# Performance work log

Measured on AMD Instinct MI355X. Metric: run time of the kernel, lower is better.

## Reference

```python
import jax, jax.numpy as jnp
import numpy as np

EMBED_DIM = 1024
NUM_HEADS = 16
HEAD_DIM = EMBED_DIM // NUM_HEADS  # 64
KERNEL_SIZE = 64


def apply_rotary_emb(x, freqs_cos, freqs_sin):
    # x: [B, L, H, D]; freqs: [L, D//2]
    x_r = x[..., 0::2]
    x_i = x[..., 1::2]
    cos = freqs_cos[None, :, None, :]
    sin = freqs_sin[None, :, None, :]
    out_r = x_r * cos - x_i * sin
    out_i = x_r * sin + x_i * cos
    return jnp.stack([out_r, out_i], axis=-1).reshape(x.shape)


def setup_inputs() -> dict:
    key = jax.random.key(0)
    ks = jax.random.split(key, 8)
    B, L = 4, 4096
    x = jax.random.normal(ks[0], (B, L, EMBED_DIM), dtype=jnp.float32)
    freqs_cos = jax.random.normal(ks[1], (L, HEAD_DIM // 2), dtype=jnp.float32)
    freqs_sin = jax.random.normal(ks[2], (L, HEAD_DIM // 2), dtype=jnp.float32)
    attention_mask = jnp.ones((B, L), dtype=jnp.float32)
    scale = 1.0 / np.sqrt(EMBED_DIM)
    Wqkv = jax.random.normal(ks[3], (EMBED_DIM, 3 * EMBED_DIM), dtype=jnp.float32) * scale
    bqkv = jnp.zeros((3 * EMBED_DIM,), dtype=jnp.float32)
    proj = jax.random.normal(ks[4], (NUM_HEADS, HEAD_DIM, KERNEL_SIZE), dtype=jnp.float32) / np.sqrt(HEAD_DIM)
    Wout = jax.random.normal(ks[5], (EMBED_DIM, EMBED_DIM), dtype=jnp.float32) * scale
    bout = jnp.zeros((EMBED_DIM,), dtype=jnp.float32)
    return {"x": x, "freqs_cos": freqs_cos, "freqs_sin": freqs_sin,
            "attention_mask": attention_mask, "Wqkv": Wqkv, "bqkv": bqkv,
            "proj": proj, "Wout": Wout, "bout": bout}


def reference(x, freqs_cos, freqs_sin, attention_mask, Wqkv, bqkv, proj, Wout, bout):
    B, L, E = x.shape
    H, D = NUM_HEADS, HEAD_DIM
    qkv = x @ Wqkv + bqkv  # [B, L, 3E]
    q, k, v = jnp.split(qkv, 3, axis=-1)
    q = q.reshape(B, L, H, D)
    k = k.reshape(B, L, H, D)
    v = v.reshape(B, L, H, D)
    q = apply_rotary_emb(q, freqs_cos, freqs_sin)
    k = apply_rotary_emb(k, freqs_cos, freqs_sin)
    q = q.transpose(0, 2, 1, 3)  # [B, H, L, D]
    k = k.transpose(0, 2, 1, 3)
    v = v.transpose(0, 2, 1, 3)
    q_prime = jax.nn.relu(jnp.einsum('bhld,hdm->bhlm', q, proj))
    k_prime = jax.nn.relu(jnp.einsum('bhld,hdm->bhlm', k, proj))
    mask = attention_mask[:, None, :, None]  # [B, 1, L, 1]
    k_prime = k_prime * mask
    v = v * mask
    kv = jnp.einsum('bhlm,bhld->bhmd', k_prime, v)      # [B, H, M, D]
    context = jnp.einsum('bhlm,bhmd->bhld', q_prime, kv)  # [B, H, L, D]
    k_sum = k_prime.sum(axis=2)  # [B, H, M]
    norm = jnp.einsum('bhlm,bhm->bhl', q_prime, k_sum)
    output = context / (norm[..., None] + 0.0001)
    output = output.transpose(0, 2, 1, 3).reshape(B, L, E)
    return output @ Wout + bout
```

## Files before the change

### kernel.cpp

```cpp
#include <hip/hip_runtime.h>

#define LSEQ   4096
#define ROWS   16384
#define EMBED  1024
#define NHEADS 16
#define HDIM   64
#define QKV_N  3072

typedef __attribute__((ext_vector_type(8))) short bf16x8;
typedef __attribute__((ext_vector_type(8))) unsigned short u16x8;
typedef __attribute__((ext_vector_type(4))) float f32x4;

__device__ inline unsigned short bf16_rne(float x) {
    unsigned int u = __float_as_uint(x);
    unsigned int r = (u + 0x7fffu + ((u >> 16) & 1u)) >> 16;
    return (unsigned short)r;
}
__device__ inline float bf16_to_f32(unsigned short h) {
    return __uint_as_float(((unsigned int)h) << 16);
}

__device__ __forceinline__ int swz64(int row, int s) {
    return row * 64 + ((((s >> 3) ^ (row & 7))) << 3) + (s & 7);
}

__global__ __launch_bounds__(256)
void convert_hilo(const float* __restrict__ in, unsigned short* __restrict__ hi,
                  unsigned short* __restrict__ lo, int n)
{
    int i = (blockIdx.x * 256 + threadIdx.x) << 2;
    if (i >= n) return;
    float4 v = *reinterpret_cast<const float4*>(&in[i]);
    float a[4] = {v.x, v.y, v.z, v.w};
    unsigned short hh[4], ll[4];
    #pragma unroll
    for (int j = 0; j < 4; ++j) {
        hh[j] = bf16_rne(a[j]);
        ll[j] = bf16_rne(a[j] - bf16_to_f32(hh[j]));
    }
    *reinterpret_cast<ushort4*>(&hi[i]) = make_ushort4(hh[0], hh[1], hh[2], hh[3]);
    *reinterpret_cast<ushort4*>(&lo[i]) = make_ushort4(ll[0], ll[1], ll[2], ll[3]);
}

__global__ __launch_bounds__(256)
void convert_T_hilo(const float* __restrict__ in, unsigned short* __restrict__ hi,
                    unsigned short* __restrict__ lo, int K, int N)
{
    __shared__ float tile[64][65];
    const int n0 = blockIdx.x * 64, k0 = blockIdx.y * 64;
    const int t = threadIdx.x;
    #pragma unroll
    for (int i = 0; i < 16; ++i) {
        int idx = t + i * 256;
        int r = idx >> 6, c = idx & 63;
        tile[r][c] = in[(size_t)(k0 + r) * N + n0 + c];
    }
    __syncthreads();
    #pragma unroll
    for (int i = 0; i < 16; ++i) {
        int idx = t + i * 256;
        int r = idx >> 6, c = idx & 63;
        float v = tile[c][r];
        unsigned short h = bf16_rne(v);
        unsigned short l = bf16_rne(v - bf16_to_f32(h));
        size_t o = (size_t)(n0 + r) * K + k0 + c;
        hi[o] = h;
        lo[o] = l;
    }
}

__global__ __launch_bounds__(512)
void gemm3_kernel(const unsigned short* __restrict__ Ah, const unsigned short* __restrict__ Al,
                  const unsigned short* __restrict__ Bh, const unsigned short* __restrict__ Bl,
                  const float* __restrict__ bias, float* __restrict__ C,
                  int K, int ldc)
{
    __shared__ __align__(16) unsigned short lds[2][32768];

    const int t = threadIdx.x;
    const int wave = t >> 6, lane = t & 63;
    const int wr = wave >> 2, wc = wave & 3;
    const int fr = lane & 15, fq = lane >> 4;

    const int nwg = gridDim.x * gridDim.y;
    const int wg  = blockIdx.y * gridDim.x + blockIdx.x;
    const int swz = (wg & 7) * (nwg >> 3) + (wg >> 3);
    const int bx = swz % gridDim.x, by = swz / gridDim.x;
    const int rowBase = by * 256;
    const int colBase = bx * 256;

    const int op = wave >> 1;
    const unsigned short* src = (op == 0) ? Ah : (op == 1) ? Al : (op == 2) ? Bh : Bl;
    const int tileRow0 = ((wave < 4) ? rowBase : colBase) + (wave & 1) * 128;
    const int subOff = op * 8192 + (wave & 1) * 4096;
    const int sRow = lane >> 2;
    const int sChunk = (((lane & 3) ^ ((lane >> 3) & 3)) << 3);

    f32x4 acc[8][4] = {};
    const int NT = K >> 5;

    #pragma unroll
    for (int i = 0; i < 8; ++i) {
        const unsigned short* g = src + (size_t)(tileRow0 + i * 16 + sRow) * K + sChunk;
        __builtin_amdgcn_global_load_lds(
            (const __attribute__((address_space(1))) void*)g,
            (__attribute__((address_space(3))) void*)&lds[0][subOff + i * 512], 16, 0, 0);
    }
    __syncthreads();

    for (int tI = 0; tI < NT; ++tI) {
        const int cur = tI & 1;
        const unsigned short* ldsC = lds[cur];
        const int k0 = (tI + 1) << 5;
        const bool pref = (tI + 1 < NT);

        bf16x8 bhf[4], blf[4];

        #pragma unroll
        for (int p = 0; p < 4; ++p) {
            if (pref && p < 2) {
                const int i0 = p * 4;
                #pragma unroll
                for (int i = 0; i < 4; ++i) {
                    const unsigned short* g =
                        src + (size_t)(tileRow0 + (i0 + i) * 16 + sRow) * K + k0 + sChunk;
                    __builtin_amdgcn_global_load_lds(
                        (const __attribute__((address_space(1))) void*)g,
                        (__attribute__((address_space(3))) void*)&lds[cur ^ 1][subOff + (i0 + i) * 512], 16, 0, 0);
                }
            }

            bf16x8 ahf[2], alf[2];
            #pragma unroll
            for (int mm = 0; mm < 2; ++mm) {
                int m = p * 2 + mm;
                int r = wr * 128 + m * 16 + fr;
                int off = r * 32 + ((fq ^ ((r >> 1) & 3)) << 3);
                ahf[mm] = *reinterpret_cast<const bf16x8*>(&ldsC[off]);
                alf[mm] = *reinterpret_cast<const bf16x8*>(&ldsC[8192 + off]);
            }
            if (p == 0) {
                #pragma unroll
                for (int n = 0; n < 4; ++n) {
                    int rb = wc * 64 + n * 16 + fr;
                    int off = rb * 32 + ((fq ^ ((rb >> 1) & 3)) << 3);
                    bhf[n] = *reinterpret_cast<const bf16x8*>(&ldsC[16384 + off]);
                    blf[n] = *reinterpret_cast<const bf16x8*>(&ldsC[24576 + off]);
                }
            }

            __builtin_amdgcn_s_barrier();
            asm volatile("s_waitcnt lgkmcnt(0)" ::: "memory");
            __builtin_amdgcn_sched_barrier(0);
            __builtin_amdgcn_s_setprio(1);
            #pragma unroll
            for (int mm = 0; mm < 2; ++mm) {
                int m = p * 2 + mm;
                #pragma unroll
                for (int n = 0; n < 4; ++n) {
                    acc[m][n] = __builtin_amdgcn_mfma_f32_16x16x32_bf16(ahf[mm], bhf[n], acc[m][n], 0, 0, 0);
                    acc[m][n] = __builtin_amdgcn_mfma_f32_16x16x32_bf16(ahf[mm], blf[n], acc[m][n], 0, 0, 0);
                    acc[m][n] = __builtin_amdgcn_mfma_f32_16x16x32_bf16(alf[mm], bhf[n], acc[m][n], 0, 0, 0);
                }
            }
            __builtin_amdgcn_s_setprio(0);
            if (p == 3)
                asm volatile("s_waitcnt vmcnt(0)" ::: "memory");
            __builtin_amdgcn_s_barrier();
        }
    }

    #pragma unroll
    for (int m = 0; m < 8; ++m) {
        #pragma unroll
        for (int n = 0; n < 4; ++n) {
            int col = colBase + wc * 64 + n * 16 + fr;
            float bv = bias[col];
            #pragma unroll
            for (int r = 0; r < 4; ++r) {
                int row = rowBase + wr * 128 + m * 16 + fq * 4 + r;
                C[(size_t)row * ldc + col] = acc[m][n][r] + bv;
            }
        }
    }
}

__global__ __launch_bounds__(256)
void kv_mfma_kernel(const float* __restrict__ kvb, const float* __restrict__ cosb,
                    const float* __restrict__ sinb, const float* __restrict__ maskb,
                    const float* __restrict__ proj, float* __restrict__ partial)
{
    __shared__ __align__(16) char smem[66816];
    unsigned short* KR_h  = (unsigned short*)smem;
    unsigned short* KR_l  = (unsigned short*)(smem + 8192);
    float*          PS    = (float*)smem;
    unsigned short* PJT_h = (unsigned short*)(smem + 16384);
    unsigned short* PJT_l = (unsigned short*)(smem + 24576);
    unsigned short* KPT_h = (unsigned short*)(smem + 32768);
    unsigned short* KPT_l = (unsigned short*)(smem + 40960);
    unsigned short* VT_h  = (unsigned short*)(smem + 49152);
    unsigned short* VT_l  = (unsigned short*)(smem + 57344);
    float*          MS    = (float*)(smem + 65536);
    float*          KS    = (float*)(smem + 65792);

    const int chunk = blockIdx.x;
    const int hh    = blockIdx.y;
    const int t = threadIdx.x;
    const int w = t >> 6, lane = t & 63;
    const int fr = lane & 15, fq = lane >> 4;

    {
        int r = t >> 2, c0 = (t & 3) << 4;
        #pragma unroll
        for (int k = 0; k < 4; ++k)
            *reinterpret_cast<float4*>(&PS[r * 64 + c0 + k * 4]) =
                *reinterpret_cast<const float4*>(&proj[(size_t)hh * 4096 + r * 64 + c0 + k * 4]);
    }
    __syncthreads();
    {
        int m = t >> 2, d0 = (t & 3) << 4;
        unsigned short hb[16], lb[16];
        #pragma unroll
        for (int j = 0; j < 16; ++j) {
            float v = PS[(d0 + j) * 64 + m];
            hb[j] = bf16_rne(v);
            lb[j] = bf16_rne(v - bf16_to_f32(hb[j]));
        }
        #pragma unroll
        for (int cp = 0; cp < 2; ++cp) {
            u16x8 vh, vl;
            #pragma unroll
            for (int j = 0; j < 8; ++j) { vh[j] = hb[cp * 8 + j]; vl[j] = lb[cp * 8 + j]; }
            int sidx = swz64(m, d0 + cp * 8);
            *reinterpret_cast<u16x8*>(&PJT_h[sidx]) = vh;
            *reinterpret_cast<u16x8*>(&PJT_l[sidx]) = vl;
        }
    }
    __syncthreads();

    f32x4 acc2[4] = {};
    float ksacc[4] = {0.f, 0.f, 0.f, 0.f};

    for (int sub = 0; sub < 4; ++sub) {
        const int rowL = chunk * 256 + sub * 64;

        float4 vv[4];
        {
            int l = t >> 2, c0 = (t & 3) << 4;
            #pragma unroll
            for (int k2 = 0; k2 < 4; ++k2)
                vv[k2] = *reinterpret_cast<const float4*>(
                    &kvb[(size_t)(rowL + l) * 2048 + 1024 + hh * 64 + c0 + k2 * 4]);
        }
        #pragma unroll
        for (int i = 0; i < 8; ++i) {
            int p = t + (i << 8);
            int l = p >> 5, i2 = p & 31;
            size_t base = (size_t)(rowL + l) * 2048 + hh * 64 + 2 * i2;
            float kr = kvb[base], ki = kvb[base + 1];
            int crow = (rowL + l) & 4095;
            float c = cosb[(size_t)crow * 32 + i2];
            float s = sinb[(size_t)crow * 32 + i2];
            float xr = kr * c - ki * s;
            float xi = kr * s + ki * c;
            unsigned short h0 = bf16_rne(xr), h1 = bf16_rne(xi);
            unsigned short l0 = bf16_rne(xr - bf16_to_f32(h0));
            unsigned short l1 = bf16_rne(xi - bf16_to_f32(h1));
            int sidx = swz64(l, 2 * i2);
            *reinterpret_cast<unsigned int*>(&KR_h[sidx]) = (unsigned)h0 | ((unsigned)h1 << 16);
            *reinterpret_cast<unsigned int*>(&KR_l[sidx]) = (unsigned)l0 | ((unsigned)l1 << 16);
        }
        if (t < 64) MS[t] = maskb[rowL + t];
        __syncthreads();

        f32x4 acc1[4] = {};
        #pragma unroll
        for (int ks = 0; ks < 2; ++ks) {
            bf16x8 ah = *reinterpret_cast<const bf16x8*>(&KR_h[swz64(16 * w + fr, ks * 32 + fq * 8)]);
            bf16x8 al = *reinterpret_cast<const bf16x8*>(&KR_l[swz64(16 * w + fr, ks * 32 + fq * 8)]);
            #pragma unroll
            for (int n = 0; n < 4; ++n) {
                bf16x8 bh = *reinterpret_cast<const bf16x8*>(&PJT_h[swz64(16 * n + fr, ks * 32 + fq * 8)]);
                bf16x8 bl = *reinterpret_cast<const bf16x8*>(&PJT_l[swz64(16 * n + fr, ks * 32 + fq * 8)]);
                acc1[n] = __builtin_amdgcn_mfma_f32_16x16x32_bf16(ah, bh, acc1[n], 0, 0, 0);
                acc1[n] = __builtin_amdgcn_mfma_f32_16x16x32_bf16(ah, bl, acc1[n], 0, 0, 0);
                acc1[n] = __builtin_amdgcn_mfma_f32_16x16x32_bf16(al, bh, acc1[n], 0, 0, 0);
            }
        }
        #pragma unroll
        for (int n = 0; n < 4; ++n) {
            unsigned short hb[4], lb[4];
            float ssum = 0.f;
            #pragma unroll
            for (int r = 0; r < 4; ++r) {
                int l = 16 * w + fq * 4 + r;
                float kp = fmaxf(acc1[n][r], 0.f) * MS[l];
                ssum += kp;
                hb[r] = bf16_rne(kp);
                lb[r] = bf16_rne(kp - bf16_to_f32(hb[r]));
            }
            ksacc[n] += ssum;
            int sidx = swz64(16 * n + fr, 16 * w + fq * 4);
            *reinterpret_cast<ushort4*>(&KPT_h[sidx]) = make_ushort4(hb[0], hb[1], hb[2], hb[3]);
            *reinterpret_cast<ushort4*>(&KPT_l[sidx]) = make_ushort4(lb[0], lb[1], lb[2], lb[3]);
        }
        __syncthreads();

        {
            float* VS = PS;
            int l = t >> 2, c0 = (t & 3) << 4;
            float mv = MS[l];
            #pragma unroll
            for (int k2 = 0; k2 < 4; ++k2) {
                float4 q = vv[k2];
                q.x *= mv; q.y *= mv; q.z *= mv; q.w *= mv;
                *reinterpret_cast<float4*>(&VS[l * 64 + c0 + k2 * 4]) = q;
            }
        }
        __syncthreads();

        {
            float* VS = PS;
            int d = t >> 2, l0 = (t & 3) << 4;
            unsigned short hb[16], lb[16];
            #pragma unroll
            for (int j = 0; j < 16; ++j) {
                float v = VS[(l0 + j) * 64 + d];
                hb[j] = bf16_rne(v);
                lb[j] = bf16_rne(v - bf16_to_f32(hb[j]));
            }
            #pragma unroll
            for (int cp = 0; cp < 2; ++cp) {
                u16x8 vh, vl;
                #pragma unroll
                for (int j = 0; j < 8; ++j) { vh[j] = hb[cp * 8 + j]; vl[j] = lb[cp * 8 + j]; }
                int sidx = swz64(d, l0 + cp * 8);
                *reinterpret_cast<u16x8*>(&VT_h[sidx]) = vh;
                *reinterpret_cast<u16x8*>(&VT_l[sidx]) = vl;
            }
        }
        __syncthreads();

        #pragma unroll
        for (int ks = 0; ks < 2; ++ks) {
            bf16x8 ah = *reinterpret_cast<const bf16x8*>(&KPT_h[swz64(16 * w + fr, ks * 32 + fq * 8)]);
            bf16x8 al = *reinterpret_cast<const bf16x8*>(&KPT_l[swz64(16 * w + fr, ks * 32 + fq * 8)]);
            #pragma unroll
            for (int n = 0; n < 4; ++n) {
                bf16x8 bh = *reinterpret_cast<const bf16x8*>(&VT_h[swz64(16 * n + fr, ks * 32 + fq * 8)]);
                bf16x8 bl = *reinterpret_cast<const bf16x8*>(&VT_l[swz64(16 * n + fr, ks * 32 + fq * 8)]);
                acc2[n] = __builtin_amdgcn_mfma_f32_16x16x32_bf16(ah, bh, acc2[n], 0, 0, 0);
                acc2[n] = __builtin_amdgcn_mfma_f32_16x16x32_bf16(ah, bl, acc2[n], 0, 0, 0);
                acc2[n] = __builtin_amdgcn_mfma_f32_16x16x32_bf16(al, bh, acc2[n], 0, 0, 0);
            }
        }
    }

    #pragma unroll
    for (int n = 0; n < 4; ++n) {
        float v = ksacc[n];
        v += __shfl_xor(v, 16);
        v += __shfl_xor(v, 32);
        if (fq == 0) KS[w * 64 + 16 * n + fr] = v;
    }
    __syncthreads();

    float* dst = partial + ((size_t)hh * 64 + chunk) * 4160;
    #pragma unroll
    for (int n = 0; n < 4; ++n)
        #pragma unroll
        for (int r = 0; r < 4; ++r) {
            int m = 16 * w + fq * 4 + r;
            int d = 16 * n + fr;
            dst[m * 64 + d] = acc2[n][r];
        }
    if (t < 64)
        dst[4096 + t] = KS[t] + KS[64 + t] + KS[128 + t] + KS[192 + t];
}

__global__ __launch_bounds__(256)
void kv_reduce_kernel(const float* __restrict__ partial, float* __restrict__ kvout)
{
    const int bh = blockIdx.x;
    const int b = bh >> 4, h = bh & 15;
    const int seg = blockIdx.y;
    for (int idx = seg * 1040 + threadIdx.x; idx < (seg + 1) * 1040; idx += 256) {
        float s = 0.f;
        for (int c = 0; c < 16; ++c)
            s += partial[((size_t)h * 64 + b * 16 + c) * 4160 + idx];
        kvout[(size_t)bh * 4160 + idx] = s;
    }
}

__global__ __launch_bounds__(256)
void context_kernel(const float* __restrict__ qb, const float* __restrict__ cosb,
                    const float* __restrict__ sinb, const float* __restrict__ proj,
                    const float* __restrict__ kvsum, unsigned short* __restrict__ ch,
                    unsigned short* __restrict__ cl)
{
    const int lt = blockIdx.x;
    const int h  = blockIdx.y;
    const int t = threadIdx.x;
    const int bh = (lt >> 6) * 16 + h;

    __shared__ float bufA[64][68];
    __shared__ float qp[64][68];
    __shared__ float pj[64][64];
    __shared__ float ksum[64];

    for (int i = t; i < 1024; i += 256)
        *reinterpret_cast<float4*>(&pj[0][0] + (size_t)i * 4) =
            *reinterpret_cast<const float4*>(proj + (size_t)h * 4096 + (size_t)i * 4);
    if (t < 64) ksum[t] = kvsum[(size_t)bh * 4160 + 4096 + t];

    const int rowL = lt * 64;
    #pragma unroll
    for (int i = 0; i < 8; ++i) {
        int p = t + i * 256;
        int l = p >> 5, i2 = p & 31;
        size_t base = (size_t)(rowL + l) * 1024 + h * HDIM + 2 * i2;
        float qr = qb[base], qi = qb[base + 1];
        int crow = (rowL + l) & 4095;
        float c = cosb[(size_t)crow * 32 + i2];
        float s = sinb[(size_t)crow * 32 + i2];
        bufA[l][2 * i2]     = qr * c - qi * s;
        bufA[l][2 * i2 + 1] = qr * s + qi * c;
    }
    __syncthreads();

    {
        int l = t >> 2, m0 = (t & 3) << 4;
        float a[16] = {};
        for (int d = 0; d < 64; ++d) {
            float ql = bufA[l][d];
            const float* pr = &pj[d][m0];
            #pragma unroll
            for (int j = 0; j < 16; ++j) a[j] = fmaf(ql, pr[j], a[j]);
        }
        #pragma unroll
        for (int j = 0; j < 16; ++j) qp[l][m0 + j] = fmaxf(a[j], 0.f);
    }
    __syncthreads();

    #pragma unroll
    for (int i = 0; i < 4; ++i) {
        int idx = t + i * 256;
        int mm = idx >> 4, dd = (idx & 15) << 2;
        *reinterpret_cast<float4*>(&bufA[mm][dd]) =
            *reinterpret_cast<const float4*>(&kvsum[(size_t)bh * 4160 + mm * 64 + dd]);
    }
    __syncthreads();

    {
        int l = t >> 2, d0 = (t & 3) << 4;
        float a[16] = {};
        float nrm = 0.f;
        for (int mm = 0; mm < 64; ++mm) {
            float qv = qp[l][mm];
            nrm = fmaf(qv, ksum[mm], nrm);
            const float* kr = &bufA[mm][d0];
            #pragma unroll
            for (int j = 0; j < 16; ++j) a[j] = fmaf(qv, kr[j], a[j]);
        }
        float inv = 1.0f / (nrm + 1e-4f);
        size_t orow = (size_t)(rowL + l) * 1024 + h * HDIM + d0;
        #pragma unroll
        for (int j4 = 0; j4 < 4; ++j4) {
            unsigned short hh2[4], ll2[4];
            #pragma unroll
            for (int j = 0; j < 4; ++j) {
                float v = a[j4 * 4 + j] * inv;
                hh2[j] = bf16_rne(v);
                ll2[j] = bf16_rne(v - bf16_to_f32(hh2[j]));
            }
            *reinterpret_cast<ushort4*>(&ch[orow + j4 * 4]) = make_ushort4(hh2[0], hh2[1], hh2[2], hh2[3]);
            *reinterpret_cast<ushort4*>(&cl[orow + j4 * 4]) = make_ushort4(ll2[0], ll2[1], ll2[2], ll2[3]);
        }
    }
}

extern "C" void kernel_launch(void* const* d_in, const int* in_sizes, int n_in,
                              void* d_out, int out_size, void* d_ws, size_t ws_size,
                              hipStream_t stream)
{
    const float* x    = (const float*)d_in[0];
    const float* fcos = (const float*)d_in[1];
    const float* fsin = (const float*)d_in[2];
    const float* mask = (const float*)d_in[3];
    const float* Wqkv = (const float*)d_in[4];
    const float* bqkv = (const float*)d_in[5];
    const float* proj = (const float*)d_in[6];
    const float* Wout = (const float*)d_in[7];
    const float* bout = (const float*)d_in[8];
    float* out = (float*)d_out;

    float* W    = (float*)d_ws;
    float* XHL  = W + 4194304;
    float* KVQ  = XHL + 16777216;
    float* PART = KVQ + 33554432;
    float* KSUM = PART + 4259840;

    unsigned short* Wqh = (unsigned short*)W;
    unsigned short* Wql = Wqh + 3145728;
    unsigned short* Woh = Wql + 3145728;
    unsigned short* Wol = Woh + 1048576;
    unsigned short* xh  = (unsigned short*)XHL;
    unsigned short* xl  = xh + 16777216;

    convert_T_hilo<<<dim3(3072 / 64, 1024 / 64), 256, 0, stream>>>(Wqkv, Wqh, Wql, 1024, 3072);
    convert_T_hilo<<<dim3(1024 / 64, 1024 / 64), 256, 0, stream>>>(Wout, Woh, Wol, 1024, 1024);

    convert_hilo<<<16384, 256, 0, stream>>>(x, xh, xl, ROWS * EMBED);

    gemm3_kernel<<<dim3(2048 / 256, ROWS / 256), 512, 0, stream>>>(
        xh, xl, Wqh + (size_t)1024 * 1024, Wql + (size_t)1024 * 1024,
        bqkv + 1024, KVQ, 1024, 2048);

    kv_mfma_kernel<<<dim3(64, 16), 256, 0, stream>>>(KVQ, fcos, fsin, mask, proj, PART);

    kv_reduce_kernel<<<dim3(64, 4), 256, 0, stream>>>(PART, KSUM);

    gemm3_kernel<<<dim3(1024 / 256, ROWS / 256), 512, 0, stream>>>(
        xh, xl, Wqh, Wql, bqkv, KVQ, 1024, 1024);

    context_kernel<<<dim3(256, 16), 256, 0, stream>>>(
        KVQ, fcos, fsin, proj, KSUM, xh, xl);

    gemm3_kernel<<<dim3(1024 / 256, ROWS / 256), 512, 0, stream>>>(
        xh, xl, Woh, Wol, bout, out, 1024, 1024);
}
```

Baseline: 505.1 us.

## Restagger GEMM prefetch across phases and drop per-phase trailing barrier

Reorganises the double-buffered global-to-LDS prefetch in the bf16 split GEMM. A-operand waves now issue two loads per phase and B-operand waves issue all eight at the first phase. Each wave gets its own s_waitcnt vmcnt threshold merged into a single barrier per phase, and the trailing barrier after the MFMA block is removed. The goal is to cut barrier stalls and spread memory traffic more evenly against MFMA work. In exchange the prefetch becomes unconditional, so the last iteration issues a redundant reload of column 0. The partial vmcnt waits also make the read/write ordering on the LDS buffers subtler and riskier.

```diff
diff --git a/kernel.cpp b/kernel.cpp
--- a/kernel.cpp
+++ b/kernel.cpp
@@ -90,8 +90,9 @@
     const int colBase = bx * 256;
 
     const int op = wave >> 1;
+    const bool isA = (wave < 4);
     const unsigned short* src = (op == 0) ? Ah : (op == 1) ? Al : (op == 2) ? Bh : Bl;
-    const int tileRow0 = ((wave < 4) ? rowBase : colBase) + (wave & 1) * 128;
+    const int tileRow0 = (isA ? rowBase : colBase) + (wave & 1) * 128;
     const int subOff = op * 8192 + (wave & 1) * 4096;
     const int sRow = lane >> 2;
     const int sChunk = (((lane & 3) ^ ((lane >> 3) & 3)) << 3);
@@ -111,25 +112,12 @@
     for (int tI = 0; tI < NT; ++tI) {
         const int cur = tI & 1;
         const unsigned short* ldsC = lds[cur];
-        const int k0 = (tI + 1) << 5;
-        const bool pref = (tI + 1 < NT);
+        const int kn = ((tI + 1 < NT) ? (tI + 1) : 0) << 5;
 
         bf16x8 bhf[4], blf[4];
 
         #pragma unroll
         for (int p = 0; p < 4; ++p) {
-            if (pref && p < 2) {
-                const int i0 = p * 4;
-                #pragma unroll
-                for (int i = 0; i < 4; ++i) {
-                    const unsigned short* g =
-                        src + (size_t)(tileRow0 + (i0 + i) * 16 + sRow) * K + k0 + sChunk;
-                    __builtin_amdgcn_global_load_lds(
-                        (const __attribute__((address_space(1))) void*)g,
-                        (__attribute__((address_space(3))) void*)&lds[cur ^ 1][subOff + (i0 + i) * 512], 16, 0, 0);
-                }
-            }
-
             bf16x8 ahf[2], alf[2];
             #pragma unroll
             for (int mm = 0; mm < 2; ++mm) {
@@ -149,9 +137,38 @@
                 }
             }
 
+            if (isA) {
+                #pragma unroll
+                for (int i = 0; i < 2; ++i) {
+                    const int ii = p * 2 + i;
+                    const unsigned short* g =
+                        src + (size_t)(tileRow0 + ii * 16 + sRow) * K + kn + sChunk;
+                    __builtin_amdgcn_global_load_lds(
+                        (const __attribute__((address_space(1))) void*)g,
+                        (__attribute__((address_space(3))) void*)&lds[cur ^ 1][subOff + ii * 512], 16, 0, 0);
+                }
+            } else if (p == 0) {
+                #pragma unroll
+                for (int ii = 0; ii < 8; ++ii) {
+                    const unsigned short* g =
+                        src + (size_t)(tileRow0 + ii * 16 + sRow) * K + kn + sChunk;
+                    __builtin_amdgcn_global_load_lds(
+                        (const __attribute__((address_space(1))) void*)g,
+                        (__attribute__((address_space(3))) void*)&lds[cur ^ 1][subOff + ii * 512], 16, 0, 0);
+                }
+            }
+
+            __builtin_amdgcn_sched_barrier(0);
+            if (isA) {
+                asm volatile("s_waitcnt vmcnt(6) lgkmcnt(0)" ::: "memory");
+            } else if (p == 3) {
+                asm volatile("s_waitcnt vmcnt(0) lgkmcnt(0)" ::: "memory");
+            } else {
+                asm volatile("s_waitcnt lgkmcnt(0)" ::: "memory");
+            }
             __builtin_amdgcn_s_barrier();
-            asm volatile("s_waitcnt lgkmcnt(0)" ::: "memory");
             __builtin_amdgcn_sched_barrier(0);
+
             __builtin_amdgcn_s_setprio(1);
             #pragma unroll
             for (int mm = 0; mm < 2; ++mm) {
@@ -164,9 +181,6 @@
                 }
             }
             __builtin_amdgcn_s_setprio(0);
-            if (p == 3)
-                asm volatile("s_waitcnt vmcnt(0)" ::: "memory");
-            __builtin_amdgcn_s_barrier();
         }
     }
 
```

Measured after the change: 501.8 us (median of 2 runs). About the same (-0.6%).

## Register double-buffer A fragments and drop per-phase barriers in split-bf16 GEMM

Applied to the files above, without the earlier changes.

Restructures the GEMM main loop. All global-to-LDS prefetches for the next K tile are issued up front, and the A fragments are double-buffered in registers so the next phase's LDS reads overlap the current MFMAs. The four per-phase s_barrier and waitcnt pairs are replaced by a single __syncthreads per K tile. The last tile now issues a redundant prefetch of tile 0 so the loop body has no branch, which costs extra loads. Removing the explicit sched_barrier leaves the overlap up to the compiler.

```diff
diff --git a/kernel.cpp b/kernel.cpp
--- a/kernel.cpp
+++ b/kernel.cpp
@@ -111,63 +111,62 @@
     for (int tI = 0; tI < NT; ++tI) {
         const int cur = tI & 1;
         const unsigned short* ldsC = lds[cur];
-        const int k0 = (tI + 1) << 5;
-        const bool pref = (tI + 1 < NT);
+        const int kn = ((tI + 1 < NT) ? (tI + 1) : 0) << 5;
+
+        #pragma unroll
+        for (int i = 0; i < 8; ++i) {
+            const unsigned short* g =
+                src + (size_t)(tileRow0 + i * 16 + sRow) * K + kn + sChunk;
+            __builtin_amdgcn_global_load_lds(
+                (const __attribute__((address_space(1))) void*)g,
+                (__attribute__((address_space(3))) void*)&lds[cur ^ 1][subOff + i * 512], 16, 0, 0);
+        }
 
         bf16x8 bhf[4], blf[4];
+        #pragma unroll
+        for (int n = 0; n < 4; ++n) {
+            int rb = wc * 64 + n * 16 + fr;
+            int off = rb * 32 + ((fq ^ ((rb >> 1) & 3)) << 3);
+            bhf[n] = *reinterpret_cast<const bf16x8*>(&ldsC[16384 + off]);
+            blf[n] = *reinterpret_cast<const bf16x8*>(&ldsC[24576 + off]);
+        }
+        bf16x8 ahf[2][2], alf[2][2];
+        #pragma unroll
+        for (int mm = 0; mm < 2; ++mm) {
+            int r = wr * 128 + mm * 16 + fr;
+            int off = r * 32 + ((fq ^ ((r >> 1) & 3)) << 3);
+            ahf[0][mm] = *reinterpret_cast<const bf16x8*>(&ldsC[off]);
+            alf[0][mm] = *reinterpret_cast<const bf16x8*>(&ldsC[8192 + off]);
+        }
 
         #pragma unroll
         for (int p = 0; p < 4; ++p) {
-            if (pref && p < 2) {
-                const int i0 = p * 4;
+            const int cb = p & 1, nb = cb ^ 1;
+            if (p < 3) {
                 #pragma unroll
-                for (int i = 0; i < 4; ++i) {
-                    const unsigned short* g =
-                        src + (size_t)(tileRow0 + (i0 + i) * 16 + sRow) * K + k0 + sChunk;
-                    __builtin_amdgcn_global_load_lds(
-                        (const __attribute__((address_space(1))) void*)g,
-                        (__attribute__((address_space(3))) void*)&lds[cur ^ 1][subOff + (i0 + i) * 512], 16, 0, 0);
+                for (int mm = 0; mm < 2; ++mm) {
+                    int m = (p + 1) * 2 + mm;
+                    int r = wr * 128 + m * 16 + fr;
+                    int off = r * 32 + ((fq ^ ((r >> 1) & 3)) << 3);
+                    ahf[nb][mm] = *reinterpret_cast<const bf16x8*>(&ldsC[off]);
+                    alf[nb][mm] = *reinterpret_cast<const bf16x8*>(&ldsC[8192 + off]);
                 }
             }
-
-            bf16x8 ahf[2], alf[2];
-            #pragma unroll
-            for (int mm = 0; mm < 2; ++mm) {
-                int m = p * 2 + mm;
-                int r = wr * 128 + m * 16 + fr;
-                int off = r * 32 + ((fq ^ ((r >> 1) & 3)) << 3);
-                ahf[mm] = *reinterpret_cast<const bf16x8*>(&ldsC[off]);
-                alf[mm] = *reinterpret_cast<const bf16x8*>(&ldsC[8192 + off]);
-            }
-            if (p == 0) {
-                #pragma unroll
-                for (int n = 0; n < 4; ++n) {
-                    int rb = wc * 64 + n * 16 + fr;
-                    int off = rb * 32 + ((fq ^ ((rb >> 1) & 3)) << 3);
-                    bhf[n] = *reinterpret_cast<const bf16x8*>(&ldsC[16384 + off]);
-                    blf[n] = *reinterpret_cast<const bf16x8*>(&ldsC[24576 + off]);
-                }
-            }
-
-            __builtin_amdgcn_s_barrier();
-            asm volatile("s_waitcnt lgkmcnt(0)" ::: "memory");
-            __builtin_amdgcn_sched_barrier(0);
             __builtin_amdgcn_s_setprio(1);
             #pragma unroll
             for (int mm = 0; mm < 2; ++mm) {
                 int m = p * 2 + mm;
                 #pragma unroll
                 for (int n = 0; n < 4; ++n) {
-                    acc[m][n] = __builtin_amdgcn_mfma_f32_16x16x32_bf16(ahf[mm], bhf[n], acc[m][n], 0, 0, 0);
-                    acc[m][n] = __builtin_amdgcn_mfma_f32_16x16x32_bf16(ahf[mm], blf[n], acc[m][n], 0, 0, 0);
-                    acc[m][n] = __builtin_amdgcn_mfma_f32_16x16x32_bf16(alf[mm], bhf[n], acc[m][n], 0, 0, 0);
+                    acc[m][n] = __builtin_amdgcn_mfma_f32_16x16x32_bf16(ahf[cb][mm], bhf[n], acc[m][n], 0, 0, 0);
+                    acc[m][n] = __builtin_amdgcn_mfma_f32_16x16x32_bf16(ahf[cb][mm], blf[n], acc[m][n], 0, 0, 0);
+                    acc[m][n] = __builtin_amdgcn_mfma_f32_16x16x32_bf16(alf[cb][mm], bhf[n], acc[m][n], 0, 0, 0);
                 }
             }
             __builtin_amdgcn_s_setprio(0);
-            if (p == 3)
-                asm volatile("s_waitcnt vmcnt(0)" ::: "memory");
-            __builtin_amdgcn_s_barrier();
-        }
+        }
+
+        __syncthreads();
     }
 
     #pragma unroll
```

Result: no change. 499.0 us (-1.2%).
